# Performance work log

Measured on AMD Instinct MI355X. Metric: run time of the kernel, lower is better.

Reference implementation:

```python
import jax, jax.numpy as jnp
import numpy as np

B, N, D = 256, 131072, 256
TEMP = 0.05
EPS_SM = 1e-6
EPS_LOG = 1e-6
NUM_CLUSTERS = 1000


def _l2norm(x):
    return x / jnp.linalg.norm(x, axis=-1, keepdims=True)


def setup_inputs() -> dict:
    key = jax.random.key(0)
    k1, k2, k3, k4, k5 = jax.random.split(key, 5)
    # re-ID features are L2-normalized in practice; keeps exp(logits/temp) finite
    inputs = _l2norm(jax.random.normal(k1, (B, D), jnp.float32))
    indexes = jax.random.randint(k2, (B,), 0, N)
    labels = jax.random.randint(k3, (N,), 0, NUM_CLUSTERS)  # pseudo cluster ids buffer
    cluster_features = _l2norm(jax.random.normal(k4, (N, D), jnp.float32))
    instance_features = _l2norm(jax.random.normal(k5, (N, D), jnp.float32))
    return {
        "inputs": inputs,
        "cluster_features": cluster_features,
        "instance_features": instance_features,
        "indexes": indexes,
        "labels": labels,
    }


def reference(inputs, cluster_features, instance_features, indexes, labels):
    # targets = labels[indexes]
    targets = labels[indexes]
    # bank similarity GEMM, temperature scaling
    logits = jnp.matmul(inputs, cluster_features.T) / TEMP  # [B, N]
    # module's custom softmax: exp / (sum + eps)  (intentionally no max-subtract)
    exps = jnp.exp(logits)
    masked_sim = exps / (jnp.sum(exps, axis=1, keepdims=True) + EPS_SM)
    logp = jnp.log(masked_sim + EPS_LOG)
    # F.nll_loss: mean of -logp at target column
    loss = -jnp.mean(jnp.take_along_axis(logp, targets[:, None], axis=1))
    return loss
```

## Files before the change

### kernel.cpp

```cpp
#include <hip/hip_runtime.h>
#include <hip/hip_bf16.h>
#include <cstdint>

#define B_ 256
#define N_ 131072
#define D_ 256
#define INV_TEMP 20.0f
#define EPS_SM 1e-6f
#define EPS_LOG 1e-6f

#define BN 128
#define BK 64
#define LDA 72
#define LDB 72
#define NSLOT 32

typedef __bf16 bf16_t;
typedef bf16_t bf16x8 __attribute__((ext_vector_type(8)));
typedef float f32x4 __attribute__((ext_vector_type(4)));

__device__ inline ushort f2bf(float f) {
  uint32_t u = __builtin_bit_cast(uint32_t, f);
  u += 0x7FFFu + ((u >> 16) & 1u);
  return (ushort)(u >> 16);
}

__global__ __launch_bounds__(256, 2)
void gemm_rowsum(const float* __restrict__ inp, const float* __restrict__ cf,
                 float* __restrict__ rowsum) {
  __shared__ ushort As[256 * LDA];
  __shared__ ushort Bs[BN * LDB];
  const int tid  = threadIdx.x;
  const int wave = tid >> 6;
  const int lane = tid & 63;
  const int m15  = lane & 15;
  const int q    = lane >> 4;
  const int n0   = blockIdx.x * BN;

  f32x4 acc[4][8];
#pragma unroll
  for (int i = 0; i < 4; ++i)
#pragma unroll
    for (int j = 0; j < 8; ++j) acc[i][j] = (f32x4){0.f, 0.f, 0.f, 0.f};

  for (int kt = 0; kt < D_; kt += BK) {
#pragma unroll
    for (int j = 0; j < 16; ++j) {
      int i = j * 256 + tid;
      int row = i >> 4, c4 = i & 15;
      const float4 v = *(const float4*)(inp + row * D_ + kt + c4 * 4);
      ushort4 w = {f2bf(v.x), f2bf(v.y), f2bf(v.z), f2bf(v.w)};
      *(ushort4*)(&As[row * LDA + c4 * 4]) = w;
    }
#pragma unroll
    for (int j = 0; j < 8; ++j) {
      int i = j * 256 + tid;
      int row = i >> 4, c4 = i & 15;
      const float4 v = *(const float4*)(cf + (size_t)(n0 + row) * D_ + kt + c4 * 4);
      ushort4 w = {f2bf(v.x), f2bf(v.y), f2bf(v.z), f2bf(v.w)};
      *(ushort4*)(&Bs[row * LDB + c4 * 4]) = w;
    }
    __syncthreads();
#pragma unroll
    for (int ks = 0; ks < 2; ++ks) {
      bf16x8 af[4], bfr[8];
#pragma unroll
      for (int mb = 0; mb < 4; ++mb)
        af[mb] = __builtin_bit_cast(
            bf16x8, *(const uint4*)(&As[(wave * 64 + mb * 16 + m15) * LDA + ks * 32 + q * 8]));
#pragma unroll
      for (int nb = 0; nb < 8; ++nb)
        bfr[nb] = __builtin_bit_cast(
            bf16x8, *(const uint4*)(&Bs[(nb * 16 + m15) * LDB + ks * 32 + q * 8]));
#pragma unroll
      for (int mb = 0; mb < 4; ++mb)
#pragma unroll
        for (int nb = 0; nb < 8; ++nb)
          acc[mb][nb] = __builtin_amdgcn_mfma_f32_16x16x32_bf16(af[mb], bfr[nb], acc[mb][nb], 0, 0, 0);
    }
    __syncthreads();
  }

  float rp[4][4];
#pragma unroll
  for (int mb = 0; mb < 4; ++mb)
#pragma unroll
    for (int r = 0; r < 4; ++r) rp[mb][r] = 0.f;
#pragma unroll
  for (int mb = 0; mb < 4; ++mb)
#pragma unroll
    for (int nb = 0; nb < 8; ++nb)
#pragma unroll
      for (int r = 0; r < 4; ++r)
        rp[mb][r] += __expf(acc[mb][nb][r] * INV_TEMP);
#pragma unroll
  for (int off = 8; off >= 1; off >>= 1)
#pragma unroll
    for (int mb = 0; mb < 4; ++mb)
#pragma unroll
      for (int r = 0; r < 4; ++r)
        rp[mb][r] += __shfl_xor(rp[mb][r], off, 64);

  if (m15 == 0) {
    float* slot = rowsum + (blockIdx.x & (NSLOT - 1)) * B_;
#pragma unroll
    for (int mb = 0; mb < 4; ++mb)
#pragma unroll
      for (int r = 0; r < 4; ++r)
        atomicAdd(&slot[wave * 64 + mb * 16 + q * 4 + r], rp[mb][r]);
  }
}

__global__ __launch_bounds__(256)
void finalize_loss(const float* __restrict__ inp, const float* __restrict__ cf,
                   const int* __restrict__ idx, const int* __restrict__ lab,
                   const float* __restrict__ rowsum, float* __restrict__ out) {
  __shared__ float red[256];
  const int b = threadIdx.x;
  const int t = lab[idx[b]];
  const float4* a = (const float4*)(inp + b * D_);
  const float4* c = (const float4*)(cf + (size_t)t * D_);
  float dot = 0.f;
#pragma unroll 8
  for (int i = 0; i < 64; ++i) {
    float4 x = a[i], y = c[i];
    dot += x.x * y.x + x.y * y.y + x.z * y.z + x.w * y.w;
  }
  float S = 0.f;
#pragma unroll
  for (int s = 0; s < NSLOT; ++s) S += rowsum[s * B_ + b];
  float logp = __logf(__expf(dot * INV_TEMP) / (S + EPS_SM) + EPS_LOG);
  red[b] = logp;
  __syncthreads();
  for (int off = 128; off >= 1; off >>= 1) {
    if (b < off) red[b] += red[b + off];
    __syncthreads();
  }
  if (b == 0) out[0] = -red[0] * (1.0f / 256.0f);
}

extern "C" void kernel_launch(void* const* d_in, const int* in_sizes, int n_in,
                              void* d_out, int out_size, void* d_ws, size_t ws_size,
                              hipStream_t stream) {
  const float* inp = (const float*)d_in[0];
  const float* cf  = (const float*)d_in[1];
  const int* idx = (const int*)d_in[3];
  const int* lab = (const int*)d_in[4];
  float* out = (float*)d_out;
  float* rowsum = (float*)d_ws;

  hipMemsetAsync(rowsum, 0, NSLOT * B_ * sizeof(float), stream);
  gemm_rowsum<<<dim3(N_ / BN), dim3(256), 0, stream>>>(inp, cf, rowsum);
  finalize_loss<<<dim3(1), dim3(256), 0, stream>>>(inp, cf, idx, lab, rowsum, out);
}
```

Before: 343.1 us.

## Keep A in registers, double-buffer B tiles, process four N tiles per block

The GEMM kernel now loads and converts the input matrix once per block into registers, using 512 threads with 8 waves of 32 rows each. It then streams four 128-column tiles of cluster features through a double-buffered LDS pipeline with register prefetch two chunks ahead, which removes the repeated per-block conversion of A and overlaps global loads with MFMA work. The exp row-sums are accumulated per tile and reduced once, and the grid shrinks by four. The finalize kernel splits each dot product over four threads. In exchange, register pressure rises (A fragments plus double-buffered loads) and there are fewer blocks.

```diff
diff --git a/kernel.cpp b/kernel.cpp
--- a/kernel.cpp
+++ b/kernel.cpp
@@ -9,10 +9,12 @@
 #define EPS_SM 1e-6f
 #define EPS_LOG 1e-6f
 
+#define TPB 512
 #define BN 128
 #define BK 64
-#define LDA 72
+#define TILES 4
 #define LDB 72
+#define BUFE (BN * LDB)
 #define NSLOT 32
 
 typedef __bf16 bf16_t;
@@ -25,118 +27,166 @@
   return (ushort)(u >> 16);
 }
 
-__global__ __launch_bounds__(256, 2)
+__global__ __launch_bounds__(TPB, 2)
 void gemm_rowsum(const float* __restrict__ inp, const float* __restrict__ cf,
                  float* __restrict__ rowsum) {
-  __shared__ ushort As[256 * LDA];
-  __shared__ ushort Bs[BN * LDB];
+  __shared__ ushort smem[2 * BUFE];
   const int tid  = threadIdx.x;
   const int wave = tid >> 6;
   const int lane = tid & 63;
   const int m15  = lane & 15;
   const int q    = lane >> 4;
-  const int n0   = blockIdx.x * BN;
-
-  f32x4 acc[4][8];
-#pragma unroll
-  for (int i = 0; i < 4; ++i)
-#pragma unroll
-    for (int j = 0; j < 8; ++j) acc[i][j] = (f32x4){0.f, 0.f, 0.f, 0.f};
-
-  for (int kt = 0; kt < D_; kt += BK) {
-#pragma unroll
-    for (int j = 0; j < 16; ++j) {
-      int i = j * 256 + tid;
-      int row = i >> 4, c4 = i & 15;
-      const float4 v = *(const float4*)(inp + row * D_ + kt + c4 * 4);
+
+  bf16x8 areg[8][2];
+#pragma unroll
+  for (int kc = 0; kc < 4; ++kc) {
+    const int row = tid >> 1, half = tid & 1;
+    const float* src = inp + row * D_ + kc * BK + half * 32;
+#pragma unroll
+    for (int i = 0; i < 8; ++i) {
+      const float4 v = *(const float4*)(src + i * 4);
       ushort4 w = {f2bf(v.x), f2bf(v.y), f2bf(v.z), f2bf(v.w)};
-      *(ushort4*)(&As[row * LDA + c4 * 4]) = w;
-    }
-#pragma unroll
-    for (int j = 0; j < 8; ++j) {
-      int i = j * 256 + tid;
-      int row = i >> 4, c4 = i & 15;
-      const float4 v = *(const float4*)(cf + (size_t)(n0 + row) * D_ + kt + c4 * 4);
+      *(ushort4*)(&smem[row * LDB + half * 32 + i * 4]) = w;
+    }
+    __syncthreads();
+#pragma unroll
+    for (int mb = 0; mb < 2; ++mb)
+#pragma unroll
+      for (int ks = 0; ks < 2; ++ks)
+        areg[kc * 2 + ks][mb] = __builtin_bit_cast(
+            bf16x8, *(const uint4*)(&smem[(wave * 32 + mb * 16 + m15) * LDB + ks * 32 + q * 8]));
+    __syncthreads();
+  }
+
+  const size_t nbase = (size_t)blockIdx.x * (TILES * BN);
+  const int brow = tid >> 2, bcg = tid & 3;
+
+  f32x4 acc[2][8];
+  float rs[2][4];
+#pragma unroll
+  for (int mb = 0; mb < 2; ++mb) {
+#pragma unroll
+    for (int nb = 0; nb < 8; ++nb) acc[mb][nb] = (f32x4){0.f, 0.f, 0.f, 0.f};
+#pragma unroll
+    for (int r = 0; r < 4; ++r) rs[mb][r] = 0.f;
+  }
+
+  float4 ldbuf[2][4];
+#define LDADDR(c) (cf + (nbase + (size_t)((c) >> 2) * BN + brow) * D_ + ((c) & 3) * BK + bcg * 16)
+
+#pragma unroll
+  for (int i = 0; i < 4; ++i) ldbuf[0][i] = *(const float4*)(LDADDR(0) + i * 4);
+#pragma unroll
+  for (int i = 0; i < 4; ++i) ldbuf[1][i] = *(const float4*)(LDADDR(1) + i * 4);
+  {
+    ushort* dst = &smem[0 * BUFE + brow * LDB + bcg * 16];
+#pragma unroll
+    for (int i = 0; i < 4; ++i) {
+      const float4 v = ldbuf[0][i];
       ushort4 w = {f2bf(v.x), f2bf(v.y), f2bf(v.z), f2bf(v.w)};
-      *(ushort4*)(&Bs[row * LDB + c4 * 4]) = w;
-    }
-    __syncthreads();
+      *(ushort4*)(dst + i * 4) = w;
+    }
+  }
+
+#pragma unroll
+  for (int c = 0; c < TILES * 4; ++c) {
+    __syncthreads();
+    if (c + 2 < TILES * 4) {
+#pragma unroll
+      for (int i = 0; i < 4; ++i) ldbuf[c & 1][i] = *(const float4*)(LDADDR(c + 2) + i * 4);
+    }
+    const ushort* bs = &smem[(c & 1) * BUFE];
 #pragma unroll
     for (int ks = 0; ks < 2; ++ks) {
-      bf16x8 af[4], bfr[8];
-#pragma unroll
-      for (int mb = 0; mb < 4; ++mb)
-        af[mb] = __builtin_bit_cast(
-            bf16x8, *(const uint4*)(&As[(wave * 64 + mb * 16 + m15) * LDA + ks * 32 + q * 8]));
+      bf16x8 bfr[8];
 #pragma unroll
       for (int nb = 0; nb < 8; ++nb)
         bfr[nb] = __builtin_bit_cast(
-            bf16x8, *(const uint4*)(&Bs[(nb * 16 + m15) * LDB + ks * 32 + q * 8]));
-#pragma unroll
-      for (int mb = 0; mb < 4; ++mb)
+            bf16x8, *(const uint4*)(&bs[(nb * 16 + m15) * LDB + ks * 32 + q * 8]));
+#pragma unroll
+      for (int mb = 0; mb < 2; ++mb)
 #pragma unroll
         for (int nb = 0; nb < 8; ++nb)
-          acc[mb][nb] = __builtin_amdgcn_mfma_f32_16x16x32_bf16(af[mb], bfr[nb], acc[mb][nb], 0, 0, 0);
-    }
-    __syncthreads();
-  }
-
-  float rp[4][4];
-#pragma unroll
-  for (int mb = 0; mb < 4; ++mb)
-#pragma unroll
-    for (int r = 0; r < 4; ++r) rp[mb][r] = 0.f;
-#pragma unroll
-  for (int mb = 0; mb < 4; ++mb)
-#pragma unroll
-    for (int nb = 0; nb < 8; ++nb)
+          acc[mb][nb] = __builtin_amdgcn_mfma_f32_16x16x32_bf16(
+              areg[(c & 3) * 2 + ks][mb], bfr[nb], acc[mb][nb], 0, 0, 0);
+    }
+    if ((c & 3) == 3) {
+#pragma unroll
+      for (int mb = 0; mb < 2; ++mb)
+#pragma unroll
+        for (int nb = 0; nb < 8; ++nb)
+#pragma unroll
+          for (int r = 0; r < 4; ++r)
+            rs[mb][r] += __expf(acc[mb][nb][r] * INV_TEMP);
+      if (c + 1 < TILES * 4) {
+#pragma unroll
+        for (int mb = 0; mb < 2; ++mb)
+#pragma unroll
+          for (int nb = 0; nb < 8; ++nb) acc[mb][nb] = (f32x4){0.f, 0.f, 0.f, 0.f};
+      }
+    }
+    if (c + 1 < TILES * 4) {
+      ushort* dst = &smem[((c + 1) & 1) * BUFE + brow * LDB + bcg * 16];
+#pragma unroll
+      for (int i = 0; i < 4; ++i) {
+        const float4 v = ldbuf[(c + 1) & 1][i];
+        ushort4 w = {f2bf(v.x), f2bf(v.y), f2bf(v.z), f2bf(v.w)};
+        *(ushort4*)(dst + i * 4) = w;
+      }
+    }
+  }
+
+#pragma unroll
+  for (int off = 8; off >= 1; off >>= 1)
+#pragma unroll
+    for (int mb = 0; mb < 2; ++mb)
 #pragma unroll
       for (int r = 0; r < 4; ++r)
-        rp[mb][r] += __expf(acc[mb][nb][r] * INV_TEMP);
-#pragma unroll
-  for (int off = 8; off >= 1; off >>= 1)
-#pragma unroll
-    for (int mb = 0; mb < 4; ++mb)
-#pragma unroll
-      for (int r = 0; r < 4; ++r)
-        rp[mb][r] += __shfl_xor(rp[mb][r], off, 64);
+        rs[mb][r] += __shfl_xor(rs[mb][r], off, 64);
 
   if (m15 == 0) {
     float* slot = rowsum + (blockIdx.x & (NSLOT - 1)) * B_;
 #pragma unroll
-    for (int mb = 0; mb < 4; ++mb)
+    for (int mb = 0; mb < 2; ++mb)
 #pragma unroll
       for (int r = 0; r < 4; ++r)
-        atomicAdd(&slot[wave * 64 + mb * 16 + q * 4 + r], rp[mb][r]);
-  }
-}
-
-__global__ __launch_bounds__(256)
+        atomicAdd(&slot[wave * 32 + mb * 16 + q * 4 + r], rs[mb][r]);
+  }
+#undef LDADDR
+}
+
+__global__ __launch_bounds__(1024)
 void finalize_loss(const float* __restrict__ inp, const float* __restrict__ cf,
                    const int* __restrict__ idx, const int* __restrict__ lab,
                    const float* __restrict__ rowsum, float* __restrict__ out) {
-  __shared__ float red[256];
-  const int b = threadIdx.x;
+  __shared__ float red[1024];
+  __shared__ float lg[256];
+  const int tid = threadIdx.x;
+  const int b = tid >> 2, part = tid & 3;
   const int t = lab[idx[b]];
-  const float4* a = (const float4*)(inp + b * D_);
-  const float4* c = (const float4*)(cf + (size_t)t * D_);
+  const float4* a = (const float4*)(inp + b * D_ + part * 64);
+  const float4* c = (const float4*)(cf + (size_t)t * D_ + part * 64);
   float dot = 0.f;
-#pragma unroll 8
-  for (int i = 0; i < 64; ++i) {
-    float4 x = a[i], y = c[i];
+#pragma unroll
+  for (int i = 0; i < 16; ++i) {
+    const float4 x = a[i], y = c[i];
     dot += x.x * y.x + x.y * y.y + x.z * y.z + x.w * y.w;
   }
-  float S = 0.f;
-#pragma unroll
-  for (int s = 0; s < NSLOT; ++s) S += rowsum[s * B_ + b];
-  float logp = __logf(__expf(dot * INV_TEMP) / (S + EPS_SM) + EPS_LOG);
-  red[b] = logp;
+  red[tid] = dot;
+  __syncthreads();
+  if (tid < 256) {
+    const float d = red[tid * 4] + red[tid * 4 + 1] + red[tid * 4 + 2] + red[tid * 4 + 3];
+    float S = 0.f;
+#pragma unroll
+    for (int s = 0; s < NSLOT; ++s) S += rowsum[s * B_ + tid];
+    lg[tid] = __logf(__expf(d * INV_TEMP) / (S + EPS_SM) + EPS_LOG);
+  }
   __syncthreads();
   for (int off = 128; off >= 1; off >>= 1) {
-    if (b < off) red[b] += red[b + off];
-    __syncthreads();
-  }
-  if (b == 0) out[0] = -red[0] * (1.0f / 256.0f);
+    if (tid < off) lg[tid] += lg[tid + off];
+    __syncthreads();
+  }
+  if (tid == 0) out[0] = -lg[0] * (1.0f / 256.0f);
 }
 
 extern "C" void kernel_launch(void* const* d_in, const int* in_sizes, int n_in,
@@ -150,6 +200,6 @@
   float* rowsum = (float*)d_ws;
 
   hipMemsetAsync(rowsum, 0, NSLOT * B_ * sizeof(float), stream);
-  gemm_rowsum<<<dim3(N_ / BN), dim3(256), 0, stream>>>(inp, cf, rowsum);
-  finalize_loss<<<dim3(1), dim3(256), 0, stream>>>(inp, cf, idx, lab, rowsum, out);
-}
+  gemm_rowsum<<<dim3(N_ / (TILES * BN)), dim3(TPB), 0, stream>>>(inp, cf, rowsum);
+  finalize_loss<<<dim3(1), dim3(1024), 0, stream>>>(inp, cf, idx, lab, rowsum, out);
+}
```

After: 287.8 us. 1.19x faster.
